# Performance work log

Hardware: AMD Instinct MI355X
Metric: run time of the kernel (lower is better)

Reference implementation:

```python
import jax, jax.numpy as jnp
import numpy as np

P, G, F, H = 128, 256, 1024, 512
EPS = 1e-5

def _bn(x, g, b, m, v):
    # eval-mode BatchNorm1d over last dim
    return (x - m) / jnp.sqrt(v + EPS) * g + b

def _lrelu(x):
    return jnp.where(x > 0, x, 0.1 * x)

def setup_inputs():
    key = jax.random.key(0)
    ks = iter(jax.random.split(key, 64))
    rn = lambda s, sc=1.0: jax.random.normal(next(ks), s, dtype=jnp.float32) * sc
    ru = lambda s: jax.random.uniform(next(ks), s, dtype=jnp.float32) + 0.5
    return {
        "f_p": rn((P, F)), "f_g": rn((G, F)),
        "bn_g": ru((F,)), "bn_b": rn((F,), 0.1), "bn_m": rn((F,), 0.1), "bn_v": ru((F,)),
        "rf_W1": rn((F, F), 0.02), "rf_b1": rn((F,), 0.01),
        "rf1_g": ru((F,)), "rf1_b": rn((F,), 0.1), "rf1_m": rn((F,), 0.1), "rf1_v": ru((F,)),
        "rf_W2": rn((F, F), 0.02), "rf_b2": rn((F,), 0.01),
        "rf2_g": ru((F,)), "rf2_b": rn((F,), 0.1), "rf2_m": rn((F,), 0.1), "rf2_v": ru((F,)),
        "sfc_W": rn((F, H), 0.02), "sfc_b": rn((H,), 0.01),
        "sbn_g": ru((H,)), "sbn_b": rn((H,), 0.1), "sbn_m": rn((H,), 0.1), "sbn_v": ru((H,)),
        "scl_W": rn((H, 1), 0.001), "scl_b": rn((1,), 0.001),
        "ffc_W": rn((F, H), 0.02), "ffc_b": rn((H,), 0.01),
        "fbn_g": ru((H,)), "fbn_b": rn((H,), 0.1), "fbn_m": rn((H,), 0.1), "fbn_v": ru((H,)),
        "cls_W": rn((H, 1), 0.001), "cls_b": rn((1,), 0.001),
    }

def reference(f_p, f_g, bn_g, bn_b, bn_m, bn_v,
              rf_W1, rf_b1, rf1_g, rf1_b, rf1_m, rf1_v,
              rf_W2, rf_b2, rf2_g, rf2_b, rf2_m, rf2_v,
              sfc_W, sfc_b, sbn_g, sbn_b, sbn_m, sbn_v, scl_W, scl_b,
              ffc_W, ffc_b, fbn_g, fbn_b, fbn_m, fbn_v, cls_W, cls_b):
    # Siamese difference feature for every probe-gallery pair: d [P,G,F]
    d = _bn((f_p[:, None, :] - f_g[None, :, :]) ** 2, bn_g, bn_b, bn_m, bn_v)
    h = _lrelu(_bn(d @ rf_W1 + rf_b1, rf1_g, rf1_b, rf1_m, rf1_v))
    t = _lrelu(_bn(h @ rf_W2 + rf_b2, rf2_g, rf2_b, rf2_m, rf2_v))
    # Gallery-gallery scalar affinities via Siamese FcBlock + ClassBlock: w [G,G]
    dg = _bn((f_g[:, None, :] - f_g[None, :, :]) ** 2, bn_g, bn_b, bn_m, bn_v)
    hg = _lrelu(_bn(dg @ sfc_W + sfc_b, sbn_g, sbn_b, sbn_m, sbn_v))
    w = (hg @ scl_W + scl_b)[..., 0]
    # Graph diffusion over the gallery axis: d_new = t @ w  [P,G,F]
    d_new = jnp.einsum('pgf,gh->phf', t, w)
    # Per-pair FC + classifier -> scalar score per (probe, gallery) pair
    feat = _lrelu(_bn(d_new @ ffc_W + ffc_b, fbn_g, fbn_b, fbn_m, fbn_v))
    result = (feat @ cls_W + cls_b)[..., 0]
    return result
```

## Files before the change

kernel.cpp:

```cpp
#include <hip/hip_runtime.h>


typedef __bf16 bf16;
typedef __attribute__((ext_vector_type(8))) __bf16 bf16x8;
typedef __attribute__((ext_vector_type(4))) float f32x4;

#define EPSV 1e-5f

__device__ __forceinline__ void async_load16(const bf16* g, bf16* l) {
    __builtin_amdgcn_global_load_lds(
        (const __attribute__((address_space(1))) void*)g,
        (__attribute__((address_space(3))) void*)l, 16, 0, 0);
}

__global__ __launch_bounds__(256) void prep_kernel(
    const float* __restrict__ g, const float* __restrict__ b,
    const float* __restrict__ m, const float* __restrict__ v,
    const float* __restrict__ bias, float* __restrict__ scale,
    float* __restrict__ offset, int n)
{
    int i = blockIdx.x * 256 + threadIdx.x;
    if (i >= n) return;
    float s = g[i] / sqrtf(v[i] + EPSV);
    float o = b[i] - m[i] * s;
    if (bias) o += bias[i] * s;
    scale[i] = s;
    offset[i] = o;
}

__global__ __launch_bounds__(256) void wtrans_kernel(
    const float* __restrict__ in, bf16* __restrict__ out, int K, int N)
{
    int k = blockIdx.x * 256 + threadIdx.x;
    int n = blockIdx.y;
    out[(size_t)n * K + k] = (bf16)in[(size_t)k * N + n];
}

__global__ __launch_bounds__(256) void wconv_kernel(
    const float* __restrict__ w_acc, const float* __restrict__ sclb,
    bf16* __restrict__ wT)
{
    int tid = blockIdx.x * 256 + threadIdx.x;
    int g2 = tid >> 8, g1 = tid & 255;
    int idx = ((g1 >> 4) <= (g2 >> 4)) ? (g1 * 256 + g2) : (g2 * 256 + g1);
    wT[tid] = (bf16)(w_acc[idx] + sclb[0]);
}

__global__ __launch_bounds__(256) void finout_kernel(
    const float* __restrict__ acc, const float* __restrict__ clsb,
    float* __restrict__ out)
{
    int i = blockIdx.x * 256 + threadIdx.x;
    out[i] = acc[i] + clsb[0];
}

template<bool PAIR>
__global__ __launch_bounds__(512) void gemm256(
    const bf16* __restrict__ A,
    const float* __restrict__ pairX, const float* __restrict__ pairY,
    const float* __restrict__ ps, const float* __restrict__ po,
    const bf16* __restrict__ BT,
    bf16* __restrict__ C,
    int K, int N, int rowOff,
    long long batchA, long long batchB, long long batchC,
    const float* __restrict__ scale, const float* __restrict__ offset,
    int lrelu,
    const float* __restrict__ fuseW, float* __restrict__ facc,
    long long faccStride)
{
    __shared__ bf16 As[2 * 256 * 64];
    __shared__ bf16 Bs[2 * 256 * 64];
    const int tid  = threadIdx.x;
    const int lane = tid & 63;
    const int wave = tid >> 6;
    const int wrow = wave >> 2, wcol = wave & 3;
    const int row0 = blockIdx.y * 256;
    const int col0 = blockIdx.x * 256;
    const int q = lane >> 4, l16 = lane & 15;
    const int z = blockIdx.z;

    const bf16* Ap = A + (size_t)z * (size_t)batchA;
    const bf16* Bp = BT + (size_t)z * (size_t)batchB;

    f32x4 acc[8][4];
#pragma unroll
    for (int mi = 0; mi < 8; ++mi)
#pragma unroll
        for (int ni = 0; ni < 4; ++ni)
#pragma unroll
            for (int e = 0; e < 4; ++e) acc[mi][ni][e] = 0.f;

    auto stageB = [&](int kk, bf16* dst) {
#pragma unroll
        for (int t = 0; t < 4; ++t) {
            int idx = t * 512 + tid;
            int r = idx >> 3, sch = idx & 7;
            int gch = sch ^ (r & 7);
            async_load16(Bp + (size_t)(col0 + r) * K + kk + gch * 8,
                         &dst[idx * 8]);
        }
    };
    auto stageA = [&](int kk, bf16* dst) {
        if constexpr (PAIR) {
#pragma unroll
            for (int t = 0; t < 4; ++t) {
                int c = tid + t * 512;
                int r = c >> 3, ch = c & 7;
                int gr = rowOff + row0 + r;
                const float* xp = pairX + (size_t)(gr >> 8) * K + kk + ch * 8;
                const float* yp = pairY + (size_t)(gr & 255) * K + kk + ch * 8;
                f32x4 x0 = *(const f32x4*)xp, x1 = *(const f32x4*)(xp + 4);
                f32x4 y0 = *(const f32x4*)yp, y1 = *(const f32x4*)(yp + 4);
                f32x4 sa = *(const f32x4*)(ps + kk + ch * 8);
                f32x4 sb = *(const f32x4*)(ps + kk + ch * 8 + 4);
                f32x4 oa = *(const f32x4*)(po + kk + ch * 8);
                f32x4 ob = *(const f32x4*)(po + kk + ch * 8 + 4);
                bf16x8 dv;
#pragma unroll
                for (int j = 0; j < 4; ++j) {
                    float d0 = x0[j] - y0[j];
                    float d1 = x1[j] - y1[j];
                    dv[j]     = (bf16)(d0 * d0 * sa[j] + oa[j]);
                    dv[j + 4] = (bf16)(d1 * d1 * sb[j] + ob[j]);
                }
                *(bf16x8*)&dst[r * 64 + ((ch ^ (r & 7)) * 8)] = dv;
            }
        } else {
#pragma unroll
            for (int t = 0; t < 4; ++t) {
                int idx = t * 512 + tid;
                int r = idx >> 3, sch = idx & 7;
                int gch = sch ^ (r & 7);
                async_load16(Ap + (size_t)(row0 + r) * K + kk + gch * 8,
                             &dst[idx * 8]);
            }
        }
    };

    stageA(0, As);
    stageB(0, Bs);

    int cur = 0;
    const int nt = K >> 6;
    for (int t = 0; t < nt; ++t) {
        const bool pf = (t + 1) < nt;
        if (pf) {
            stageA(t * 64 + 64, As + (cur ^ 1) * 16384);
            stageB(t * 64 + 64, Bs + (cur ^ 1) * 16384);
        }
        if (pf) {
            if constexpr (PAIR)
                asm volatile("s_waitcnt vmcnt(4) lgkmcnt(0)\n\ts_barrier"
                             ::: "memory");
            else
                asm volatile("s_waitcnt vmcnt(8)\n\ts_barrier" ::: "memory");
        } else {
            asm volatile("s_waitcnt vmcnt(0) lgkmcnt(0)\n\ts_barrier"
                         ::: "memory");
        }

        const bf16* Asb = As + cur * 16384;
        const bf16* Bsb = Bs + cur * 16384;
#pragma unroll
        for (int s = 0; s < 2; ++s) {
            bf16x8 af[8], bfr[4];
#pragma unroll
            for (int mi = 0; mi < 8; ++mi) {
                int r = wrow * 128 + mi * 16 + l16;
                af[mi] = *(const bf16x8*)&Asb[r * 64 + (((s * 4 + q) ^ (r & 7)) * 8)];
            }
#pragma unroll
            for (int ni = 0; ni < 4; ++ni) {
                int rc = wcol * 64 + ni * 16 + l16;
                bfr[ni] = *(const bf16x8*)&Bsb[rc * 64 + (((s * 4 + q) ^ (rc & 7)) * 8)];
            }
#pragma unroll
            for (int mi = 0; mi < 8; ++mi)
#pragma unroll
                for (int ni = 0; ni < 4; ++ni)
                    acc[mi][ni] = __builtin_amdgcn_mfma_f32_16x16x32_bf16(
                        af[mi], bfr[ni], acc[mi][ni], 0, 0, 0);
        }
        if (pf) asm volatile("s_barrier" ::: "memory");
        cur ^= 1;
    }

    if (fuseW) {
#pragma unroll
        for (int mi = 0; mi < 8; ++mi)
#pragma unroll
            for (int i = 0; i < 4; ++i) {
                float rs = 0.f;
#pragma unroll
                for (int ni = 0; ni < 4; ++ni) {
                    int cc = col0 + wcol * 64 + ni * 16 + l16;
                    float val = acc[mi][ni][i] * scale[cc] + offset[cc];
                    val = val > 0.f ? val : 0.1f * val;
                    rs += val * fuseW[cc];
                }
                rs += __shfl_xor(rs, 1, 64);
                rs += __shfl_xor(rs, 2, 64);
                rs += __shfl_xor(rs, 4, 64);
                rs += __shfl_xor(rs, 8, 64);
                if (l16 == 0) {
                    int r = row0 + wrow * 128 + mi * 16 + q * 4 + i;
                    atomicAdd(facc + (size_t)z * faccStride + r, rs);
                }
            }
        return;
    }
    bf16* Cp = C + (size_t)z * (size_t)batchC;
#pragma unroll
    for (int mi = 0; mi < 8; ++mi)
#pragma unroll
        for (int ni = 0; ni < 4; ++ni)
#pragma unroll
            for (int i = 0; i < 4; ++i) {
                int r = row0 + wrow * 128 + mi * 16 + q * 4 + i;
                int cc = col0 + wcol * 64 + ni * 16 + l16;
                float val = acc[mi][ni][i];
                if (scale) val = val * scale[cc] + offset[cc];
                if (lrelu) val = val > 0.f ? val : 0.1f * val;
                Cp[(size_t)r * N + cc] = (bf16)val;
            }
}

__global__ __launch_bounds__(512) void gemm_aff(
    const float* __restrict__ pairX,
    const float* __restrict__ ps, const float* __restrict__ po,
    const bf16* __restrict__ BT,
    int K,
    const float* __restrict__ scale, const float* __restrict__ offset,
    const float* __restrict__ sclW, float* __restrict__ w_acc)
{
    __shared__ bf16 As[256 * 64];
    __shared__ bf16 Bs[128 * 64];
    const int tid  = threadIdx.x;
    const int lane = tid & 63;
    const int wave = tid >> 6;
    const int wrow = wave >> 1, wcol = wave & 1;
    const int q = lane >> 4, l16 = lane & 15;
    const int col0 = blockIdx.x * 128;

    int ta = 0, rem = blockIdx.y;
    while (rem >= 16 - ta) { rem -= 16 - ta; ++ta; }
    const int tb = ta + rem;

    f32x4 acc[4][4];
#pragma unroll
    for (int mi = 0; mi < 4; ++mi)
#pragma unroll
        for (int ni = 0; ni < 4; ++ni)
#pragma unroll
            for (int e = 0; e < 4; ++e) acc[mi][ni][e] = 0.f;

    for (int kk = 0; kk < K; kk += 64) {
#pragma unroll
        for (int t = 0; t < 4; ++t) {
            int c = tid + t * 512;
            int r = c >> 3, ch = c & 7;
            int g1 = ta * 16 + (r >> 4), g2 = tb * 16 + (r & 15);
            const float* xp = pairX + (size_t)g1 * K + kk + ch * 8;
            const float* yp = pairX + (size_t)g2 * K + kk + ch * 8;
            f32x4 x0 = *(const f32x4*)xp, x1 = *(const f32x4*)(xp + 4);
            f32x4 y0 = *(const f32x4*)yp, y1 = *(const f32x4*)(yp + 4);
            f32x4 sa = *(const f32x4*)(ps + kk + ch * 8);
            f32x4 sb = *(const f32x4*)(ps + kk + ch * 8 + 4);
            f32x4 oa = *(const f32x4*)(po + kk + ch * 8);
            f32x4 ob = *(const f32x4*)(po + kk + ch * 8 + 4);
            bf16x8 dv;
#pragma unroll
            for (int j = 0; j < 4; ++j) {
                float d0 = x0[j] - y0[j];
                float d1 = x1[j] - y1[j];
                dv[j]     = (bf16)(d0 * d0 * sa[j] + oa[j]);
                dv[j + 4] = (bf16)(d1 * d1 * sb[j] + ob[j]);
            }
            *(bf16x8*)&As[r * 64 + ((ch ^ (r & 7)) * 8)] = dv;
        }
#pragma unroll
        for (int t = 0; t < 2; ++t) {
            int idx = t * 512 + tid;
            int r = idx >> 3, sch = idx & 7;
            int gch = sch ^ (r & 7);
            async_load16(BT + (size_t)(col0 + r) * K + kk + gch * 8,
                         &Bs[idx * 8]);
        }
        __syncthreads();

#pragma unroll
        for (int s = 0; s < 2; ++s) {
            bf16x8 af[4], bfr[4];
#pragma unroll
            for (int mi = 0; mi < 4; ++mi) {
                int r = wrow * 64 + mi * 16 + l16;
                af[mi] = *(const bf16x8*)&As[r * 64 + (((s * 4 + q) ^ (r & 7)) * 8)];
            }
#pragma unroll
            for (int ni = 0; ni < 4; ++ni) {
                int rc = wcol * 64 + ni * 16 + l16;
                bfr[ni] = *(const bf16x8*)&Bs[rc * 64 + (((s * 4 + q) ^ (rc & 7)) * 8)];
            }
#pragma unroll
            for (int mi = 0; mi < 4; ++mi)
#pragma unroll
                for (int ni = 0; ni < 4; ++ni)
                    acc[mi][ni] = __builtin_amdgcn_mfma_f32_16x16x32_bf16(
                        af[mi], bfr[ni], acc[mi][ni], 0, 0, 0);
        }
        __syncthreads();
    }

#pragma unroll
    for (int mi = 0; mi < 4; ++mi)
#pragma unroll
        for (int i = 0; i < 4; ++i) {
            float rs = 0.f;
#pragma unroll
            for (int ni = 0; ni < 4; ++ni) {
                int cc = col0 + wcol * 64 + ni * 16 + l16;
                float val = acc[mi][ni][i] * scale[cc] + offset[cc];
                val = val > 0.f ? val : 0.1f * val;
                rs += val * sclW[cc];
            }
            rs += __shfl_xor(rs, 1, 64);
            rs += __shfl_xor(rs, 2, 64);
            rs += __shfl_xor(rs, 4, 64);
            rs += __shfl_xor(rs, 8, 64);
            if (l16 == 0) {
                int r = wrow * 64 + mi * 16 + q * 4 + i;
                int g1 = ta * 16 + (r >> 4), g2 = tb * 16 + (r & 15);
                atomicAdd(w_acc + g1 * 256 + g2, rs);
            }
        }
}

extern "C" void kernel_launch(void* const* d_in, const int* in_sizes, int n_in,
                              void* d_out, int out_size, void* d_ws, size_t ws_size,
                              hipStream_t stream)
{
    const float* f_p   = (const float*)d_in[0];
    const float* f_g   = (const float*)d_in[1];
    const float* bn_g  = (const float*)d_in[2];
    const float* bn_b  = (const float*)d_in[3];
    const float* bn_m  = (const float*)d_in[4];
    const float* bn_v  = (const float*)d_in[5];
    const float* rf_W1 = (const float*)d_in[6];
    const float* rf_b1 = (const float*)d_in[7];
    const float* rf1_g = (const float*)d_in[8];
    const float* rf1_b = (const float*)d_in[9];
    const float* rf1_m = (const float*)d_in[10];
    const float* rf1_v = (const float*)d_in[11];
    const float* rf_W2 = (const float*)d_in[12];
    const float* rf_b2 = (const float*)d_in[13];
    const float* rf2_g = (const float*)d_in[14];
    const float* rf2_b = (const float*)d_in[15];
    const float* rf2_m = (const float*)d_in[16];
    const float* rf2_v = (const float*)d_in[17];
    const float* sfc_W = (const float*)d_in[18];
    const float* sfc_b = (const float*)d_in[19];
    const float* sbn_g = (const float*)d_in[20];
    const float* sbn_b = (const float*)d_in[21];
    const float* sbn_m = (const float*)d_in[22];
    const float* sbn_v = (const float*)d_in[23];
    const float* scl_W = (const float*)d_in[24];
    const float* scl_b = (const float*)d_in[25];
    const float* ffc_W = (const float*)d_in[26];
    const float* ffc_b = (const float*)d_in[27];
    const float* fbn_g = (const float*)d_in[28];
    const float* fbn_b = (const float*)d_in[29];
    const float* fbn_m = (const float*)d_in[30];
    const float* fbn_v = (const float*)d_in[31];
    const float* cls_W = (const float*)d_in[32];
    const float* cls_b = (const float*)d_in[33];

    const size_t MB = 1ull << 20;
    char* ws = (char*)d_ws;
    float* SC      = (float*)(ws);
    float *s0 = SC,        *o0 = SC + 1024;
    float *s1 = SC + 2048, *o1 = SC + 3072;
    float *s2 = SC + 4096, *o2 = SC + 5120;
    float *s3 = SC + 6144, *o3 = SC + 6656;
    float *s4 = SC + 7168, *o4 = SC + 7680;
    float* w_acc   = (float*)(ws + 65536);
    float* out_acc = (float*)(ws + 327680);
    bf16* wT       = (bf16*)(ws + 458752);
    bf16* W1T      = (bf16*)(ws + 1 * MB);
    bf16* W2T      = (bf16*)(ws + 3 * MB);
    bf16* sfcT     = (bf16*)(ws + 5 * MB);
    bf16* ffcT     = (bf16*)(ws + 6 * MB);

    int nc;
    if      (ws_size >= 170 * MB) nc = 1;
    else if (ws_size >= 90 * MB)  nc = 2;
    else                          nc = 4;
    const int pc = 128 / nc;
    const int R  = pc * 256;
    const size_t hbytes = (size_t)R * 1024 * 2;
    bf16* bufA = (bf16*)(ws + 8 * MB);
    bf16* bufB = (bf16*)(ws + 8 * MB + hbytes);
    bf16* bufC = (bf16*)(ws + 8 * MB + 2 * hbytes);

    prep_kernel<<<dim3(4), 256, 0, stream>>>(bn_g, bn_b, bn_m, bn_v, nullptr, s0, o0, 1024);
    prep_kernel<<<dim3(4), 256, 0, stream>>>(rf1_g, rf1_b, rf1_m, rf1_v, rf_b1, s1, o1, 1024);
    prep_kernel<<<dim3(4), 256, 0, stream>>>(rf2_g, rf2_b, rf2_m, rf2_v, rf_b2, s2, o2, 1024);
    prep_kernel<<<dim3(2), 256, 0, stream>>>(sbn_g, sbn_b, sbn_m, sbn_v, sfc_b, s3, o3, 512);
    prep_kernel<<<dim3(2), 256, 0, stream>>>(fbn_g, fbn_b, fbn_m, fbn_v, ffc_b, s4, o4, 512);

    wtrans_kernel<<<dim3(4, 1024), 256, 0, stream>>>(rf_W1, W1T, 1024, 1024);
    wtrans_kernel<<<dim3(4, 1024), 256, 0, stream>>>(rf_W2, W2T, 1024, 1024);
    wtrans_kernel<<<dim3(4, 512), 256, 0, stream>>>(sfc_W, sfcT, 1024, 512);
    wtrans_kernel<<<dim3(4, 512), 256, 0, stream>>>(ffc_W, ffcT, 1024, 512);

    hipMemsetAsync(ws + 65536, 0, 393216, stream);

    gemm_aff<<<dim3(4, 136), 512, 0, stream>>>(
        f_g, s0, o0, sfcT, 1024, s3, o3, scl_W, w_acc);
    wconv_kernel<<<dim3(256), 256, 0, stream>>>(w_acc, scl_b, wT);

    for (int ci = 0; ci < nc; ++ci) {
        gemm256<true><<<dim3(4, R / 256), 512, 0, stream>>>(
            nullptr, f_p, f_g, s0, o0, W1T, bufA, 1024, 1024, ci * R,
            0, 0, 0, s1, o1, 1, nullptr, nullptr, 0);
        gemm256<false><<<dim3(4, R / 256), 512, 0, stream>>>(
            bufA, nullptr, nullptr, nullptr, nullptr, W2T, bufB, 1024, 1024, 0,
            0, 0, 0, s2, o2, 1, nullptr, nullptr, 0);
        gemm256<false><<<dim3(1, 2, pc), 512, 0, stream>>>(
            ffcT, nullptr, nullptr, nullptr, nullptr, bufB, bufC, 1024, 256, 0,
            0, (long long)256 * 1024, (long long)512 * 256,
            nullptr, nullptr, 0, nullptr, nullptr, 0);
        gemm256<false><<<dim3(2, 1, pc), 512, 0, stream>>>(
            wT, nullptr, nullptr, nullptr, nullptr, bufC, nullptr, 256, 512, 0,
            0, (long long)512 * 256, 0,
            s4, o4, 1, cls_W, out_acc + (size_t)ci * pc * 256, 256);
    }
    finout_kernel<<<dim3(128), 256, 0, stream>>>(out_acc, cls_b, (float*)d_out);
}
```

Measured before the change: 560.9 us.

## Materialize pair-difference matrix in a separate kernel and remap GEMM workgroups for XCD locality

The squared-difference BatchNorm feature is no longer computed inside the first GEMM's A-staging loop. A new elementwise kernel writes it to a bf16 buffer, so every GEMM uses async global-to-LDS loads for A. This removes the synchronous fp32 loads and conversion work from the GEMM's main loop, at the cost of an extra write and read of the d buffer. It also adds a workgroup-index swizzle for non-batched grids that maps consecutive tiles onto the same XCD, aiming for better L2 reuse.

```diff
diff --git a/kernel.cpp b/kernel.cpp
--- a/kernel.cpp
+++ b/kernel.cpp
@@ -54,14 +54,37 @@
     out[i] = acc[i] + clsb[0];
 }
 
-template<bool PAIR>
+__global__ __launch_bounds__(256) void dprep_kernel(
+    const float* __restrict__ X, const float* __restrict__ Y,
+    const float* __restrict__ ps, const float* __restrict__ po,
+    bf16* __restrict__ d, int rowOff)
+{
+    int t  = blockIdx.x * 256 + threadIdx.x;
+    int k0 = (t & 127) * 8;
+    int r  = t >> 7;
+    int gr = rowOff + r;
+    const float* xp = X + (size_t)(gr >> 8) * 1024 + k0;
+    const float* yp = Y + (size_t)(gr & 255) * 1024 + k0;
+    f32x4 x0 = *(const f32x4*)xp, x1 = *(const f32x4*)(xp + 4);
+    f32x4 y0 = *(const f32x4*)yp, y1 = *(const f32x4*)(yp + 4);
+    f32x4 sa = *(const f32x4*)(ps + k0), sb = *(const f32x4*)(ps + k0 + 4);
+    f32x4 oa = *(const f32x4*)(po + k0), ob = *(const f32x4*)(po + k0 + 4);
+    bf16x8 dv;
+#pragma unroll
+    for (int j = 0; j < 4; ++j) {
+        float d0 = x0[j] - y0[j];
+        float d1 = x1[j] - y1[j];
+        dv[j]     = (bf16)(d0 * d0 * sa[j] + oa[j]);
+        dv[j + 4] = (bf16)(d1 * d1 * sb[j] + ob[j]);
+    }
+    *(bf16x8*)&d[(size_t)r * 1024 + k0] = dv;
+}
+
 __global__ __launch_bounds__(512) void gemm256(
     const bf16* __restrict__ A,
-    const float* __restrict__ pairX, const float* __restrict__ pairY,
-    const float* __restrict__ ps, const float* __restrict__ po,
     const bf16* __restrict__ BT,
     bf16* __restrict__ C,
-    int K, int N, int rowOff,
+    int K, int N,
     long long batchA, long long batchB, long long batchC,
     const float* __restrict__ scale, const float* __restrict__ offset,
     int lrelu,
@@ -74,11 +97,23 @@
     const int lane = tid & 63;
     const int wave = tid >> 6;
     const int wrow = wave >> 2, wcol = wave & 3;
-    const int row0 = blockIdx.y * 256;
-    const int col0 = blockIdx.x * 256;
     const int q = lane >> 4, l16 = lane & 15;
     const int z = blockIdx.z;
 
+    int bx = blockIdx.x, by = blockIdx.y;
+    {
+        int nwg = gridDim.x * gridDim.y;
+        if (gridDim.z == 1 && (nwg & 7) == 0) {
+            int lin = by * gridDim.x + bx;
+            int cpx = nwg >> 3;
+            int s = (lin & 7) * cpx + (lin >> 3);
+            bx = s % gridDim.x;
+            by = s / gridDim.x;
+        }
+    }
+    const int row0 = by * 256;
+    const int col0 = bx * 256;
+
     const bf16* Ap = A + (size_t)z * (size_t)batchA;
     const bf16* Bp = BT + (size_t)z * (size_t)batchB;
 
@@ -90,6 +125,16 @@
 #pragma unroll
             for (int e = 0; e < 4; ++e) acc[mi][ni][e] = 0.f;
 
+    auto stageA = [&](int kk, bf16* dst) {
+#pragma unroll
+        for (int t = 0; t < 4; ++t) {
+            int idx = t * 512 + tid;
+            int r = idx >> 3, sch = idx & 7;
+            int gch = sch ^ (r & 7);
+            async_load16(Ap + (size_t)(row0 + r) * K + kk + gch * 8,
+                         &dst[idx * 8]);
+        }
+    };
     auto stageB = [&](int kk, bf16* dst) {
 #pragma unroll
         for (int t = 0; t < 4; ++t) {
@@ -98,42 +143,6 @@
             int gch = sch ^ (r & 7);
             async_load16(Bp + (size_t)(col0 + r) * K + kk + gch * 8,
                          &dst[idx * 8]);
-        }
-    };
-    auto stageA = [&](int kk, bf16* dst) {
-        if constexpr (PAIR) {
-#pragma unroll
-            for (int t = 0; t < 4; ++t) {
-                int c = tid + t * 512;
-                int r = c >> 3, ch = c & 7;
-                int gr = rowOff + row0 + r;
-                const float* xp = pairX + (size_t)(gr >> 8) * K + kk + ch * 8;
-                const float* yp = pairY + (size_t)(gr & 255) * K + kk + ch * 8;
-                f32x4 x0 = *(const f32x4*)xp, x1 = *(const f32x4*)(xp + 4);
-                f32x4 y0 = *(const f32x4*)yp, y1 = *(const f32x4*)(yp + 4);
-                f32x4 sa = *(const f32x4*)(ps + kk + ch * 8);
-                f32x4 sb = *(const f32x4*)(ps + kk + ch * 8 + 4);
-                f32x4 oa = *(const f32x4*)(po + kk + ch * 8);
-                f32x4 ob = *(const f32x4*)(po + kk + ch * 8 + 4);
-                bf16x8 dv;
-#pragma unroll
-                for (int j = 0; j < 4; ++j) {
-                    float d0 = x0[j] - y0[j];
-                    float d1 = x1[j] - y1[j];
-                    dv[j]     = (bf16)(d0 * d0 * sa[j] + oa[j]);
-                    dv[j + 4] = (bf16)(d1 * d1 * sb[j] + ob[j]);
-                }
-                *(bf16x8*)&dst[r * 64 + ((ch ^ (r & 7)) * 8)] = dv;
-            }
-        } else {
-#pragma unroll
-            for (int t = 0; t < 4; ++t) {
-                int idx = t * 512 + tid;
-                int r = idx >> 3, sch = idx & 7;
-                int gch = sch ^ (r & 7);
-                async_load16(Ap + (size_t)(row0 + r) * K + kk + gch * 8,
-                             &dst[idx * 8]);
-            }
         }
     };
 
@@ -149,11 +158,7 @@
             stageB(t * 64 + 64, Bs + (cur ^ 1) * 16384);
         }
         if (pf) {
-            if constexpr (PAIR)
-                asm volatile("s_waitcnt vmcnt(4) lgkmcnt(0)\n\ts_barrier"
-                             ::: "memory");
-            else
-                asm volatile("s_waitcnt vmcnt(8)\n\ts_barrier" ::: "memory");
+            asm volatile("s_waitcnt vmcnt(8)\n\ts_barrier" ::: "memory");
         } else {
             asm volatile("s_waitcnt vmcnt(0) lgkmcnt(0)\n\ts_barrier"
                          ::: "memory");
@@ -419,18 +424,20 @@
     wconv_kernel<<<dim3(256), 256, 0, stream>>>(w_acc, scl_b, wT);
 
     for (int ci = 0; ci < nc; ++ci) {
-        gemm256<true><<<dim3(4, R / 256), 512, 0, stream>>>(
-            nullptr, f_p, f_g, s0, o0, W1T, bufA, 1024, 1024, ci * R,
+        dprep_kernel<<<dim3(R / 2), 256, 0, stream>>>(
+            f_p, f_g, s0, o0, bufB, ci * R);
+        gemm256<<<dim3(4, R / 256), 512, 0, stream>>>(
+            bufB, W1T, bufA, 1024, 1024,
             0, 0, 0, s1, o1, 1, nullptr, nullptr, 0);
-        gemm256<false><<<dim3(4, R / 256), 512, 0, stream>>>(
-            bufA, nullptr, nullptr, nullptr, nullptr, W2T, bufB, 1024, 1024, 0,
+        gemm256<<<dim3(4, R / 256), 512, 0, stream>>>(
+            bufA, W2T, bufB, 1024, 1024,
             0, 0, 0, s2, o2, 1, nullptr, nullptr, 0);
-        gemm256<false><<<dim3(1, 2, pc), 512, 0, stream>>>(
-            ffcT, nullptr, nullptr, nullptr, nullptr, bufB, bufC, 1024, 256, 0,
+        gemm256<<<dim3(1, 2, pc), 512, 0, stream>>>(
+            ffcT, bufB, bufC, 1024, 256,
             0, (long long)256 * 1024, (long long)512 * 256,
             nullptr, nullptr, 0, nullptr, nullptr, 0);
-        gemm256<false><<<dim3(2, 1, pc), 512, 0, stream>>>(
-            wT, nullptr, nullptr, nullptr, nullptr, bufC, nullptr, 256, 512, 0,
+        gemm256<<<dim3(2, 1, pc), 512, 0, stream>>>(
+            wT, bufC, nullptr, 256, 512,
             0, (long long)512 * 256, 0,
             s4, o4, 1, cls_W, out_acc + (size_t)ci * pc * 256, 256);
     }
```

Result: faster. 547.7 us (-2.4%).
